# Kernel optimization log

Measured on AMD Instinct MI355X. Metric: run time of the kernel, lower is better.

Reference implementation:

```python
import jax, jax.numpy as jnp
import numpy as np

N_NODES = 50000
N_EDGES = 500000
NEG_SLOPE = 0.2


def gat_conv(h, src, dst, W, attn_l, attn_r, bias, activation):
    """DGL-style GATConv (feat_drop=attn_drop=0, no residual).
    h: [N, F_in]; W: [F_in, H*D]; attn_l/attn_r: [H, D]; bias: [H*D].
    Returns [N, H, D]."""
    H, D = attn_l.shape
    feat = (h @ W).reshape(-1, H, D)                      # [N, H, D]
    el = (feat * attn_l).sum(-1)                          # [N, H]
    er = (feat * attn_r).sum(-1)                          # [N, H]
    e = jax.nn.leaky_relu(el[src] + er[dst], NEG_SLOPE)   # [E, H] edge logits
    # edge softmax over incoming edges of each dst node
    emax = jax.ops.segment_max(e, dst, num_segments=N_NODES)
    emax = jnp.where(jnp.isfinite(emax), emax, 0.0)       # guard zero in-degree
    ee = jnp.exp(e - emax[dst])                           # [E, H]
    denom = jax.ops.segment_sum(ee, dst, num_segments=N_NODES)
    alpha = ee / jnp.maximum(denom[dst], 1e-9)            # [E, H]
    # weighted scatter-aggregate of source features
    out = jax.ops.segment_sum(feat[src] * alpha[..., None], dst,
                              num_segments=N_NODES)       # [N, H, D]
    out = out + bias.reshape(1, H, D)
    return activation(out) if activation is not None else out


def setup_inputs() -> dict:
    key = jax.random.key(0)
    ks = jax.random.split(key, 20)
    in0, in1, hid, heads, ncls = 256, 128, 64, 8, 10

    def xn(k, shape):
        fan = shape[0] + (shape[1] if len(shape) > 1 else shape[0])
        return jax.random.normal(k, shape, jnp.float32) * np.float32(np.sqrt(2.0 / fan)) * 1.414

    inp = {
        "feat0": jax.random.normal(ks[0], (30000, in0), jnp.float32),
        "feat1": jax.random.normal(ks[1], (20000, in1), jnp.float32),
        "fc0_w": xn(ks[2], (in0, hid)), "fc0_b": jnp.zeros((hid,), jnp.float32),
        "fc1_w": xn(ks[3], (in1, hid)), "fc1_b": jnp.zeros((hid,), jnp.float32),
        "W0": xn(ks[4], (hid, heads * hid)),
        "al0": xn(ks[5], (heads, hid)), "ar0": xn(ks[6], (heads, hid)),
        "b0": jnp.zeros((heads * hid,), jnp.float32),
        "W1": xn(ks[7], (heads * hid, heads * hid)),
        "al1": xn(ks[8], (heads, hid)), "ar1": xn(ks[9], (heads, hid)),
        "b1": jnp.zeros((heads * hid,), jnp.float32),
        "W2": xn(ks[10], (heads * hid, 1 * ncls)),
        "al2": xn(ks[11], (1, ncls)), "ar2": xn(ks[12], (1, ncls)),
        "b2": jnp.zeros((ncls,), jnp.float32),
        "edge_index": jax.random.randint(ks[13], (2, N_EDGES), 0, N_NODES, jnp.int64
                                         if jax.config.jax_enable_x64 else jnp.int32),
    }
    return inp


def reference(feat0, feat1, fc0_w, fc0_b, fc1_w, fc1_b,
              W0, al0, ar0, b0, W1, al1, ar1, b1, W2, al2, ar2, b2,
              edge_index):
    src, dst = edge_index[0], edge_index[1]
    # per-type linear projection then concat along node axis
    h = jnp.concatenate([feat0 @ fc0_w + fc0_b, feat1 @ fc1_w + fc1_b], axis=0)
    h = gat_conv(h, src, dst, W0, al0, ar0, b0, jax.nn.elu).reshape(N_NODES, -1)
    h = gat_conv(h, src, dst, W1, al1, ar1, b1, jax.nn.elu).reshape(N_NODES, -1)
    logits = gat_conv(h, src, dst, W2, al2, ar2, b2, None).mean(axis=1)  # [N, ncls]
    return logits
```

## Files before the change

### kernel.cpp

```cpp
#include <hip/hip_runtime.h>
#include <hip/hip_bf16.h>
#include <hip/hip_fp16.h>

#define N_NODES 50000
#define N_EDGES 500000
#define HEADS 8
#define HID 64
#define HD 512
#define NCLS 10
#define M_PAD 50048
#define YTILES 391

typedef _Float16 f16x8 __attribute__((ext_vector_type(8)));
typedef _Float16 h8v   __attribute__((ext_vector_type(8)));
typedef float    f32x4 __attribute__((ext_vector_type(4)));

#define GLD_LDS16(g, l) __builtin_amdgcn_global_load_lds( \
    (__attribute__((address_space(1))) void*)(g),         \
    (__attribute__((address_space(3))) void*)(l), 16, 0, 0)

#define T0_TILES 469
#define T1_TILES 313
__global__ __launch_bounds__(256) void fc_gemm(const float* __restrict__ A0,
                                               const float* __restrict__ B0,
                                               const float* __restrict__ bias0,
                                               const float* __restrict__ A1,
                                               const float* __restrict__ B1,
                                               const float* __restrict__ bias1,
                                               _Float16* __restrict__ Cb) {
    __shared__ float As[16][68];
    __shared__ float Bs[16][68];
    int bid = blockIdx.x;
    const float* A; const float* B; const float* bias;
    int M, K, row_off, m0;
    if (bid < T0_TILES) { A = A0; B = B0; bias = bias0; M = 30000; K = 256; row_off = 0;     m0 = bid * 64; }
    else                { A = A1; B = B1; bias = bias1; M = 20000; K = 128; row_off = 30000; m0 = (bid - T0_TILES) * 64; }
    int tid = threadIdx.x;
    int tx = tid & 15, ty = tid >> 4;
    float acc[4][4] = {};
    int arow = tid >> 2;
    int akq  = (tid & 3) * 4;
    int brow = tid >> 4;
    int bcol = (tid & 15) * 4;
    for (int k0 = 0; k0 < K; k0 += 16) {
        int m = m0 + arow;
        float4 av = make_float4(0.f, 0.f, 0.f, 0.f);
        if (m < M) av = *(const float4*)(A + (size_t)m * K + k0 + akq);
        As[akq + 0][arow] = av.x; As[akq + 1][arow] = av.y;
        As[akq + 2][arow] = av.z; As[akq + 3][arow] = av.w;
        float4 bv = *(const float4*)(B + (size_t)(k0 + brow) * 64 + bcol);
        *(float4*)(&Bs[brow][bcol]) = bv;
        __syncthreads();
#pragma unroll
        for (int k = 0; k < 16; k++) {
            float4 a = *(const float4*)(&As[k][ty * 4]);
            float4 b = *(const float4*)(&Bs[k][tx * 4]);
            float av4[4] = {a.x, a.y, a.z, a.w};
            float bv4[4] = {b.x, b.y, b.z, b.w};
#pragma unroll
            for (int i = 0; i < 4; i++)
#pragma unroll
                for (int j = 0; j < 4; j++) acc[i][j] += av4[i] * bv4[j];
        }
        __syncthreads();
    }
#pragma unroll
    for (int i = 0; i < 4; i++) {
        int m = m0 + ty * 4 + i;
        if (m < M) {
#pragma unroll
            for (int j = 0; j < 4; j++) {
                int col = tx * 4 + j;
                Cb[(size_t)(row_off + m) * 64 + col] = (_Float16)(acc[i][j] + bias[col]);
            }
        }
    }
}

#define NBLK_SCAN 196

__global__ void count_kernel(const int* __restrict__ dst, int* __restrict__ cnt) {
    int t = blockIdx.x * blockDim.x + threadIdx.x;
    if (t < N_EDGES) atomicAdd(&cnt[dst[t]], 1);
}

__global__ void scan_part(const int* __restrict__ cnt, int* __restrict__ part) {
    __shared__ int s[256];
    int i = blockIdx.x * 256 + threadIdx.x;
    s[threadIdx.x] = (i < N_NODES) ? cnt[i] : 0;
    __syncthreads();
    for (int off = 128; off; off >>= 1) {
        if (threadIdx.x < off) s[threadIdx.x] += s[threadIdx.x + off];
        __syncthreads();
    }
    if (threadIdx.x == 0) part[blockIdx.x] = s[0];
}

__global__ void scan_offs(int* __restrict__ part) {
    __shared__ int s[256];
    int tid = threadIdx.x;
    int v = (tid < NBLK_SCAN) ? part[tid] : 0;
    s[tid] = v;
    __syncthreads();
    for (int off = 1; off < 256; off <<= 1) {
        int x = (tid >= off) ? s[tid - off] : 0;
        __syncthreads();
        s[tid] += x;
        __syncthreads();
    }
    if (tid < NBLK_SCAN) part[tid] = s[tid] - v;
}

__global__ void scan_apply(const int* __restrict__ cnt, const int* __restrict__ part,
                           int* __restrict__ rp, int* __restrict__ cur) {
    __shared__ int s[256];
    int tid = threadIdx.x;
    int i = blockIdx.x * 256 + tid;
    int v = (i < N_NODES) ? cnt[i] : 0;
    s[tid] = v;
    __syncthreads();
    for (int off = 1; off < 256; off <<= 1) {
        int x = (tid >= off) ? s[tid - off] : 0;
        __syncthreads();
        s[tid] += x;
        __syncthreads();
    }
    if (i < N_NODES) {
        int excl = s[tid] - v + part[blockIdx.x];
        rp[i] = excl; cur[i] = excl;
    }
    if (i == 0) rp[N_NODES] = N_EDGES;
}

__global__ void scatter_kernel(const int* __restrict__ src, const int* __restrict__ dst,
                               int* __restrict__ cursor, int* __restrict__ src_sorted) {
    int t = blockIdx.x * blockDim.x + threadIdx.x;
    if (t >= N_EDGES) return;
    int pos = atomicAdd(&cursor[dst[t]], 1);
    src_sorted[pos] = src[t];
}

__global__ void wtrans(const float* __restrict__ W0, const float* __restrict__ W1,
                       _Float16* __restrict__ W0t, _Float16* __restrict__ W1t) {
    int t = blockIdx.x * blockDim.x + threadIdx.x;
    if (t < 64 * 512) {
        int n = t >> 6, k = t & 63;
        W0t[t] = (_Float16)W0[k * 512 + n];
    } else {
        int u = t - 64 * 512;
        if (u >= 512 * 512) return;
        int n = u >> 9, k = u & 511;
        W1t[u] = (_Float16)W1[k * 512 + n];
    }
}

__global__ __launch_bounds__(512) void gemm_mfma_wide(const _Float16* __restrict__ A,
                                                      const _Float16* __restrict__ Bt,
                                                      _Float16* __restrict__ Cb,
                                                      const float* __restrict__ al,
                                                      const float* __restrict__ ar,
                                                      float* __restrict__ el,
                                                      float* __restrict__ er,
                                                      int M, int K) {
    __shared__ _Float16 Asl[128 * 32];
    __shared__ _Float16 Bsl[256 * 32];
    int bid = blockIdx.x;
    int k8 = bid & 7, jj = bid >> 3;
    int y = k8 + 8 * (jj >> 1);
    if (y >= YTILES) return;
    int m0 = y * 128;
    int n0 = (jj & 1) * 256;
    int t = threadIdx.x;
    int lane = t & 63;
    int w = t >> 6;
    int wm = (w & 1) * 64, wn = (w >> 1) * 64;
    int l15 = lane & 15, quad = lane >> 4;
    f32x4 acc[4][4];
#pragma unroll
    for (int i = 0; i < 4; i++)
#pragma unroll
        for (int j = 0; j < 4; j++) acc[i][j] = (f32x4){0.f, 0.f, 0.f, 0.f};

    int fbA = t * 16;
    int rowA = fbA >> 6, kgA = ((fbA >> 4) & 3) ^ (rowA & 3);
    int fbB0 = t * 16;
    int fbB1 = fbB0 + 8192;
    int rowB0 = fbB0 >> 6, kgB0 = ((fbB0 >> 4) & 3) ^ (rowB0 & 3);
    int rowB1 = fbB1 >> 6, kgB1 = ((fbB1 >> 4) & 3) ^ (rowB1 & 3);

    for (int k0 = 0; k0 < K; k0 += 32) {
        GLD_LDS16(A + (size_t)(m0 + rowA) * K + k0 + kgA * 8, (char*)Asl + fbA);
        GLD_LDS16(Bt + (size_t)(n0 + rowB0) * K + k0 + kgB0 * 8, (char*)Bsl + fbB0);
        GLD_LDS16(Bt + (size_t)(n0 + rowB1) * K + k0 + kgB1 * 8, (char*)Bsl + fbB1);
        __syncthreads();
        f16x8 af[4], bfr[4];
#pragma unroll
        for (int i = 0; i < 4; i++) {
            int r = wm + i * 16 + l15;
            int kg = quad ^ (r & 3);
            af[i] = *(const f16x8*)(Asl + r * 32 + kg * 8);
        }
#pragma unroll
        for (int j = 0; j < 4; j++) {
            int r = wn + j * 16 + l15;
            int kg = quad ^ (r & 3);
            bfr[j] = *(const f16x8*)(Bsl + r * 32 + kg * 8);
        }
#pragma unroll
        for (int i = 0; i < 4; i++)
#pragma unroll
            for (int j = 0; j < 4; j++)
                acc[i][j] = __builtin_amdgcn_mfma_f32_16x16x32_f16(af[i], bfr[j], acc[i][j], 0, 0, 0);
        __syncthreads();
    }
#pragma unroll
    for (int i = 0; i < 4; i++) {
        int rbase = m0 + wm + i * 16 + quad * 4;
#pragma unroll
        for (int j = 0; j < 4; j++) {
            int col = n0 + wn + j * 16 + l15;
#pragma unroll
            for (int r = 0; r < 4; r++) {
                int row = rbase + r;
                if (row < M) Cb[(size_t)row * HD + col] = (_Float16)acc[i][j][r];
            }
        }
    }
    int h = (n0 + wn) >> 6;
    float alv[4], arv[4];
#pragma unroll
    for (int j = 0; j < 4; j++) {
        alv[j] = al[h * 64 + j * 16 + l15];
        arv[j] = ar[h * 64 + j * 16 + l15];
    }
#pragma unroll
    for (int i = 0; i < 4; i++) {
#pragma unroll
        for (int r = 0; r < 4; r++) {
            float sl = 0.f, sr = 0.f;
#pragma unroll
            for (int j = 0; j < 4; j++) {
                float v = acc[i][j][r];
                sl += v * alv[j]; sr += v * arv[j];
            }
#pragma unroll
            for (int mk = 1; mk < 16; mk <<= 1) {
                sl += __shfl_xor(sl, mk);
                sr += __shfl_xor(sr, mk);
            }
            int row = m0 + wm + i * 16 + quad * 4 + r;
            if (l15 == 0 && row < M) {
                el[row * HEADS + h] = sl;
                er[row * HEADS + h] = sr;
            }
        }
    }
}

__global__ __launch_bounds__(64) void attn_agg(
        const int* __restrict__ rp, const int* __restrict__ srcs,
        const float* __restrict__ el, const float* __restrict__ er,
        const _Float16* __restrict__ feat, const float* __restrict__ bias,
        _Float16* __restrict__ out) {
    __shared__ float aS[592];
    __shared__ int   sS[64];
    int lane = threadIdx.x;
    int n    = blockIdx.x;
    int s0 = rp[n], s1 = rp[n + 1];
    int deg = s1 - s0;
    float er8[8];
    {
        f32x4 a = *(const f32x4*)(er + (size_t)n * 8);
        f32x4 b = *(const f32x4*)(er + (size_t)n * 8 + 4);
        er8[0]=a[0]; er8[1]=a[1]; er8[2]=a[2]; er8[3]=a[3];
        er8[4]=b[0]; er8[5]=b[1]; er8[6]=b[2]; er8[7]=b[3];
    }
    bool fast = (deg <= 64);
    if (fast) {
        bool act = lane < deg;
        int sp = act ? srcs[s0 + lane] : 0;
        sS[lane] = sp;
        f32x4 ea = {0.f,0.f,0.f,0.f}, eb = {0.f,0.f,0.f,0.f};
        if (act) {
            ea = *(const f32x4*)(el + (size_t)sp * 8);
            eb = *(const f32x4*)(el + (size_t)sp * 8 + 4);
        }
        float e8[8] = {ea[0],ea[1],ea[2],ea[3],eb[0],eb[1],eb[2],eb[3]};
#pragma unroll
        for (int h = 0; h < 8; h++) {
            float e = e8[h] + er8[h];
            e = e > 0.f ? e : 0.2f * e;
            e8[h] = act ? e : -1e30f;
        }
#pragma unroll
        for (int h = 0; h < 8; h++) {
            float mm = e8[h];
#pragma unroll
            for (int mk = 1; mk < 64; mk <<= 1) mm = fmaxf(mm, __shfl_xor(mm, mk));
            float pv = act ? __expf(e8[h] - mm) : 0.f;
            float ss = pv;
#pragma unroll
            for (int mk = 1; mk < 64; mk <<= 1) ss += __shfl_xor(ss, mk);
            aS[lane * 9 + h] = pv * (1.f / fmaxf(ss, 1e-9f));
        }
    } else {
        float m8[8], s8[8];
#pragma unroll
        for (int h = 0; h < 8; h++) { m8[h] = -1e30f; s8[h] = 0.f; }
        for (int base = s0; base < s1; base += 64) {
            bool act = base + lane < s1;
            int sp = act ? srcs[base + lane] : 0;
            f32x4 ea = {0.f,0.f,0.f,0.f}, eb = {0.f,0.f,0.f,0.f};
            if (act) {
                ea = *(const f32x4*)(el + (size_t)sp * 8);
                eb = *(const f32x4*)(el + (size_t)sp * 8 + 4);
            }
            float ev[8] = {ea[0],ea[1],ea[2],ea[3],eb[0],eb[1],eb[2],eb[3]};
#pragma unroll
            for (int h = 0; h < 8; h++) {
                float e = ev[h] + er8[h];
                e = e > 0.f ? e : 0.2f * e;
                e = act ? e : -1e30f;
                float cm = e;
#pragma unroll
                for (int mk = 1; mk < 64; mk <<= 1) cm = fmaxf(cm, __shfl_xor(cm, mk));
                float nm = fmaxf(m8[h], cm);
                float pv = act ? __expf(e - nm) : 0.f;
#pragma unroll
                for (int mk = 1; mk < 64; mk <<= 1) pv += __shfl_xor(pv, mk);
                s8[h] = s8[h] * __expf(m8[h] - nm) + pv;
                m8[h] = nm;
            }
        }
        if (lane == 0) {
#pragma unroll
            for (int h = 0; h < 8; h++) {
                aS[576 + h] = 1.f / fmaxf(s8[h], 1e-9f);
                aS[584 + h] = m8[h];
            }
        }
    }
    __builtin_amdgcn_wave_barrier();
    int hh = lane >> 3, d0 = (lane & 7) * 8;
    h8v z = {(_Float16)0, (_Float16)0, (_Float16)0, (_Float16)0,
             (_Float16)0, (_Float16)0, (_Float16)0, (_Float16)0};
    h8v acc0 = z, acc1 = z, acc2 = z, acc3 = z;
    const _Float16* colbase = feat + hh * 64 + d0;
    if (fast) {
        int p = 0;
        for (; p + 4 <= deg; p += 4) {
            int spa = sS[p],     spb = sS[p + 1];
            int spc = sS[p + 2], spd = sS[p + 3];
            _Float16 aa = (_Float16)aS[p * 9 + hh];
            _Float16 ab = (_Float16)aS[(p + 1) * 9 + hh];
            _Float16 ac = (_Float16)aS[(p + 2) * 9 + hh];
            _Float16 ad = (_Float16)aS[(p + 3) * 9 + hh];
            h8v fa = *(const h8v*)(colbase + (size_t)spa * HD);
            h8v fb = *(const h8v*)(colbase + (size_t)spb * HD);
            h8v fc = *(const h8v*)(colbase + (size_t)spc * HD);
            h8v fd = *(const h8v*)(colbase + (size_t)spd * HD);
            h8v a8a = {aa, aa, aa, aa, aa, aa, aa, aa};
            h8v a8b = {ab, ab, ab, ab, ab, ab, ab, ab};
            h8v a8c = {ac, ac, ac, ac, ac, ac, ac, ac};
            h8v a8d = {ad, ad, ad, ad, ad, ad, ad, ad};
            acc0 += a8a * fa;
            acc1 += a8b * fb;
            acc2 += a8c * fc;
            acc3 += a8d * fd;
        }
        for (; p < deg; p++) {
            int sp = sS[p];
            _Float16 ah = (_Float16)aS[p * 9 + hh];
            h8v a8 = {ah, ah, ah, ah, ah, ah, ah, ah};
            h8v f = *(const h8v*)(colbase + (size_t)sp * HD);
            acc0 += a8 * f;
        }
    } else {
        float inv_l = aS[576 + hh];
        float m_l   = aS[584 + hh];
        float ern_l = er[(size_t)n * 8 + hh];
        for (int p = s0; p < s1; p++) {
            int sp = srcs[p];
            float e = el[(size_t)sp * 8 + hh] + ern_l;
            e = e > 0.f ? e : 0.2f * e;
            _Float16 ah = (_Float16)(__expf(e - m_l) * inv_l);
            h8v a8 = {ah, ah, ah, ah, ah, ah, ah, ah};
            h8v f = *(const h8v*)(colbase + (size_t)sp * HD);
            acc0 += a8 * f;
        }
    }
    acc0 += acc1; acc2 += acc3; acc0 += acc2;
    float4 b0v = *(const float4*)(bias + lane * 8);
    float4 b1v = *(const float4*)(bias + lane * 8 + 4);
    float bb[8] = {b0v.x,b0v.y,b0v.z,b0v.w,b1v.x,b1v.y,b1v.z,b1v.w};
    h8v o;
#pragma unroll
    for (int j = 0; j < 8; j++) {
        float x = (float)acc0[j] + bb[j];
        x = x > 0.f ? x : __expf(x) - 1.f;
        o[j] = (_Float16)x;
    }
    *(h8v*)(out + (size_t)n * HD + lane * 8) = o;
}

__global__ __launch_bounds__(256) void gemm_n10v2(
        const _Float16* __restrict__ A, const float* __restrict__ B,
        const float* __restrict__ al2, const float* __restrict__ ar2,
        float* __restrict__ C, float* __restrict__ el, float* __restrict__ er) {
    __shared__ float Bs[512 * 11];
    int t = threadIdx.x;
    for (int i = t; i < 512 * NCLS; i += 256) {
        int k = i / NCLS, c = i - k * NCLS;
        Bs[k * 11 + c] = B[i];
    }
    __syncthreads();
    int lane = t & 63;
    int m = blockIdx.x * 4 + (t >> 6);
    float acc[NCLS];
#pragma unroll
    for (int c = 0; c < NCLS; c++) acc[c] = 0.f;
    const _Float16* a = A + (size_t)m * HD;
#pragma unroll
    for (int j = 0; j < 8; j++) {
        float av = (float)a[j * 64 + lane];
        const float* br = Bs + (j * 64 + lane) * 11;
#pragma unroll
        for (int c = 0; c < NCLS; c++) acc[c] += av * br[c];
    }
#pragma unroll
    for (int c = 0; c < NCLS; c++)
#pragma unroll
        for (int mk = 1; mk < 64; mk <<= 1) acc[c] += __shfl_xor(acc[c], mk);
    if (lane == 0) {
        float e1 = 0.f, e2 = 0.f;
#pragma unroll
        for (int c = 0; c < NCLS; c++) { e1 += acc[c] * al2[c]; e2 += acc[c] * ar2[c]; }
        el[m] = e1; er[m] = e2;
#pragma unroll
        for (int c = 0; c < NCLS; c++) C[(size_t)m * NCLS + c] = acc[c];
    }
}

__global__ __launch_bounds__(64) void attn2_agg2(
        const int* __restrict__ rp, const int* __restrict__ srcs,
        const float* __restrict__ el, const float* __restrict__ er,
        const float* __restrict__ feat2, const float* __restrict__ b2,
        float* __restrict__ out) {
    int lane = threadIdx.x;
    int n = blockIdx.x;
    int s0 = rp[n], s1 = rp[n + 1], deg = s1 - s0;
    float ern = er[n];
    float facc[NCLS];
#pragma unroll
    for (int c = 0; c < NCLS; c++) facc[c] = 0.f;
    if (deg <= 64) {
        bool act = lane < deg;
        int sp = act ? srcs[s0 + lane] : 0;
        float e = act ? el[sp] + ern : 0.f;
        e = e > 0.f ? e : 0.2f * e;
        if (!act) e = -1e30f;
        float mm = e;
#pragma unroll
        for (int mk = 1; mk < 64; mk <<= 1) mm = fmaxf(mm, __shfl_xor(mm, mk));
        float pv = act ? __expf(e - mm) : 0.f;
        float ss = pv;
#pragma unroll
        for (int mk = 1; mk < 64; mk <<= 1) ss += __shfl_xor(ss, mk);
        float a = pv / fmaxf(ss, 1e-9f);
        if (act) {
#pragma unroll
            for (int c = 0; c < NCLS; c++) facc[c] = a * feat2[(size_t)sp * NCLS + c];
        }
    } else {
        float mm = -1e30f, ssum = 0.f;
        for (int base = s0; base < s1; base += 64) {
            bool act = base + lane < s1;
            int sp = act ? srcs[base + lane] : 0;
            float e = act ? el[sp] + ern : 0.f;
            e = e > 0.f ? e : 0.2f * e;
            if (!act) e = -1e30f;
            float cm = e;
#pragma unroll
            for (int mk = 1; mk < 64; mk <<= 1) cm = fmaxf(cm, __shfl_xor(cm, mk));
            float nm = fmaxf(mm, cm);
            float pv = act ? __expf(e - nm) : 0.f;
#pragma unroll
            for (int mk = 1; mk < 64; mk <<= 1) pv += __shfl_xor(pv, mk);
            ssum = ssum * __expf(mm - nm) + pv;
            mm = nm;
        }
        float inv = 1.f / fmaxf(ssum, 1e-9f);
        for (int base = s0; base < s1; base += 64) {
            bool act = base + lane < s1;
            int sp = act ? srcs[base + lane] : 0;
            float e = act ? el[sp] + ern : 0.f;
            e = e > 0.f ? e : 0.2f * e;
            float a = act ? __expf(e - mm) * inv : 0.f;
            if (act) {
#pragma unroll
                for (int c = 0; c < NCLS; c++) facc[c] += a * feat2[(size_t)sp * NCLS + c];
            }
        }
    }
#pragma unroll
    for (int c = 0; c < NCLS; c++)
#pragma unroll
        for (int mk = 1; mk < 64; mk <<= 1) facc[c] += __shfl_xor(facc[c], mk);
    if (lane == 0) {
#pragma unroll
        for (int c = 0; c < NCLS; c++) out[(size_t)n * NCLS + c] = facc[c] + b2[c];
    }
}

extern "C" void kernel_launch(void* const* d_in, const int* in_sizes, int n_in,
                              void* d_out, int out_size, void* d_ws, size_t ws_size,
                              hipStream_t stream) {
    const float* feat0 = (const float*)d_in[0];
    const float* feat1 = (const float*)d_in[1];
    const float* fc0_w = (const float*)d_in[2];
    const float* fc0_b = (const float*)d_in[3];
    const float* fc1_w = (const float*)d_in[4];
    const float* fc1_b = (const float*)d_in[5];
    const float* W0    = (const float*)d_in[6];
    const float* al0   = (const float*)d_in[7];
    const float* ar0   = (const float*)d_in[8];
    const float* b0    = (const float*)d_in[9];
    const float* W1    = (const float*)d_in[10];
    const float* al1   = (const float*)d_in[11];
    const float* ar1   = (const float*)d_in[12];
    const float* b1    = (const float*)d_in[13];
    const float* W2    = (const float*)d_in[14];
    const float* al2   = (const float*)d_in[15];
    const float* ar2   = (const float*)d_in[16];
    const float* b2    = (const float*)d_in[17];
    const int* eidx    = (const int*)d_in[18];
    const int* src = eidx;
    const int* dst = eidx + N_EDGES;
    float* out = (float*)d_out;

    char* ws = (char*)d_ws;
    size_t off = 0;
    auto alloc = [&](size_t bytes) { size_t o = off; off = (off + bytes + 255) & ~(size_t)255; return o; };

    _Float16* featA = (_Float16*)(ws + alloc((size_t)M_PAD * HD * 2));
    _Float16* aggh  = (_Float16*)(ws + alloc((size_t)M_PAD * HD * 2));
    _Float16* h0h   = (_Float16*)(ws + alloc((size_t)M_PAD * 64 * 2));
    float*    feat2 = (float*)(ws + alloc((size_t)N_NODES * NCLS * 4));
    float*    el    = (float*)(ws + alloc((size_t)N_NODES * HEADS * 4));
    float*    er    = (float*)(ws + alloc((size_t)N_NODES * HEADS * 4));
    float*    el2   = (float*)(ws + alloc((size_t)N_NODES * 4));
    float*    er2   = (float*)(ws + alloc((size_t)N_NODES * 4));
    int*      cnt   = (int*)  (ws + alloc((size_t)N_NODES * 4));
    int*      rp    = (int*)  (ws + alloc((size_t)(N_NODES + 1) * 4));
    int*      cur   = (int*)  (ws + alloc((size_t)N_NODES * 4));
    int*      srcs  = (int*)  (ws + alloc((size_t)N_EDGES * 4));
    int*      part  = (int*)  (ws + alloc(1024));
    _Float16* W0t   = (_Float16*)(ws + alloc(512 * 64 * 2));
    _Float16* W1t   = (_Float16*)(ws + alloc(512 * 512 * 2));

    fc_gemm<<<T0_TILES + T1_TILES, 256, 0, stream>>>(feat0, fc0_w, fc0_b,
                                                     feat1, fc1_w, fc1_b, h0h);
    wtrans<<<(64 * 512 + 512 * 512 + 255) / 256, 256, 0, stream>>>(W0, W1, W0t, W1t);

    hipMemsetAsync(cnt, 0, N_NODES * sizeof(int), stream);
    count_kernel<<<(N_EDGES + 255) / 256, 256, 0, stream>>>(dst, cnt);
    scan_part<<<NBLK_SCAN, 256, 0, stream>>>(cnt, part);
    scan_offs<<<1, 256, 0, stream>>>(part);
    scan_apply<<<NBLK_SCAN, 256, 0, stream>>>(cnt, part, rp, cur);
    scatter_kernel<<<(N_EDGES + 255) / 256, 256, 0, stream>>>(src, dst, cur, srcs);

    int ggrid = 8 * 98;

    gemm_mfma_wide<<<ggrid, 512, 0, stream>>>(h0h, W0t, featA, al0, ar0, el, er,
                                              N_NODES, 64);
    attn_agg<<<N_NODES, 64, 0, stream>>>(rp, srcs, el, er, featA, b0, aggh);

    gemm_mfma_wide<<<ggrid, 512, 0, stream>>>(aggh, W1t, featA, al1, ar1, el, er,
                                              N_NODES, HD);
    attn_agg<<<N_NODES, 64, 0, stream>>>(rp, srcs, el, er, featA, b1, aggh);

    gemm_n10v2<<<N_NODES / 4, 256, 0, stream>>>(aggh, W2, al2, ar2, feat2, el2, er2);
    attn2_agg2<<<N_NODES, 64, 0, stream>>>(rp, srcs, el2, er2, feat2, b2, out);
}
```

Before: 541.0 us.

## Fold fc projections into W0 and run layer-0 GEMM on MFMA

Precomputes fc_w·W0 (and the fc biases times W0) so the per-type input projection and the first GAT projection become one fp16 MFMA GEMM over the raw features. The scalar fp32 fc_gemm, the separate weight transpose and the memset are replaced by a single prep kernel that also converts the features to fp16 and zeroes the counts. The layer-0 GEMM now has K=256/128 instead of 64, which adds more MFMA work and a full fp16 copy of the input features. It also rounds the combined weights to fp16, which changes numerics.

```diff
diff --git a/kernel.cpp b/kernel.cpp
--- a/kernel.cpp
+++ b/kernel.cpp
@@ -9,7 +9,9 @@
 #define HD 512
 #define NCLS 10
 #define M_PAD 50048
-#define YTILES 391
+#define YTILES_L1 391
+#define F0ROWS 30080
+#define F1ROWS 20096
 
 typedef _Float16 f16x8 __attribute__((ext_vector_type(8)));
 typedef _Float16 h8v   __attribute__((ext_vector_type(8)));
@@ -19,62 +21,70 @@
     (__attribute__((address_space(1))) void*)(g),         \
     (__attribute__((address_space(3))) void*)(l), 16, 0, 0)
 
-#define T0_TILES 469
-#define T1_TILES 313
-__global__ __launch_bounds__(256) void fc_gemm(const float* __restrict__ A0,
-                                               const float* __restrict__ B0,
-                                               const float* __restrict__ bias0,
-                                               const float* __restrict__ A1,
-                                               const float* __restrict__ B1,
-                                               const float* __restrict__ bias1,
-                                               _Float16* __restrict__ Cb) {
-    __shared__ float As[16][68];
-    __shared__ float Bs[16][68];
-    int bid = blockIdx.x;
-    const float* A; const float* B; const float* bias;
-    int M, K, row_off, m0;
-    if (bid < T0_TILES) { A = A0; B = B0; bias = bias0; M = 30000; K = 256; row_off = 0;     m0 = bid * 64; }
-    else                { A = A1; B = B1; bias = bias1; M = 20000; K = 128; row_off = 30000; m0 = (bid - T0_TILES) * 64; }
-    int tid = threadIdx.x;
-    int tx = tid & 15, ty = tid >> 4;
-    float acc[4][4] = {};
-    int arow = tid >> 2;
-    int akq  = (tid & 3) * 4;
-    int brow = tid >> 4;
-    int bcol = (tid & 15) * 4;
-    for (int k0 = 0; k0 < K; k0 += 16) {
-        int m = m0 + arow;
-        float4 av = make_float4(0.f, 0.f, 0.f, 0.f);
-        if (m < M) av = *(const float4*)(A + (size_t)m * K + k0 + akq);
-        As[akq + 0][arow] = av.x; As[akq + 1][arow] = av.y;
-        As[akq + 2][arow] = av.z; As[akq + 3][arow] = av.w;
-        float4 bv = *(const float4*)(B + (size_t)(k0 + brow) * 64 + bcol);
-        *(float4*)(&Bs[brow][bcol]) = bv;
-        __syncthreads();
-#pragma unroll
-        for (int k = 0; k < 16; k++) {
-            float4 a = *(const float4*)(&As[k][ty * 4]);
-            float4 b = *(const float4*)(&Bs[k][tx * 4]);
-            float av4[4] = {a.x, a.y, a.z, a.w};
-            float bv4[4] = {b.x, b.y, b.z, b.w};
-#pragma unroll
-            for (int i = 0; i < 4; i++)
-#pragma unroll
-                for (int j = 0; j < 4; j++) acc[i][j] += av4[i] * bv4[j];
-        }
-        __syncthreads();
-    }
-#pragma unroll
-    for (int i = 0; i < 4; i++) {
-        int m = m0 + ty * 4 + i;
-        if (m < M) {
-#pragma unroll
-            for (int j = 0; j < 4; j++) {
-                int col = tx * 4 + j;
-                Cb[(size_t)(row_off + m) * 64 + col] = (_Float16)(acc[i][j] + bias[col]);
-            }
-        }
-    }
+#define E_N (F0ROWS * 256)
+#define F_N (F1ROWS * 128)
+#define A_N (512 * 256)
+#define B_N (512 * 128)
+#define C_N (512 * 512)
+#define D_N 1024
+#define PREP_TOTAL (E_N + F_N + A_N + B_N + C_N + D_N + N_NODES)
+
+__global__ void prep(const float* __restrict__ feat0, const float* __restrict__ feat1,
+                     const float* __restrict__ fc0_w, const float* __restrict__ fc0_b,
+                     const float* __restrict__ fc1_w, const float* __restrict__ fc1_b,
+                     const float* __restrict__ W0, const float* __restrict__ W1,
+                     _Float16* __restrict__ f0h, _Float16* __restrict__ f1h,
+                     _Float16* __restrict__ Wc0t, _Float16* __restrict__ Wc1t,
+                     _Float16* __restrict__ W1t, float* __restrict__ biasF,
+                     int* __restrict__ cnt) {
+    int idx = blockIdx.x * 256 + threadIdx.x;
+    if (idx < E_N) {
+        int m = idx >> 8, k = idx & 255;
+        f0h[idx] = (m < 30000) ? (_Float16)feat0[(size_t)m * 256 + k] : (_Float16)0.f;
+        return;
+    }
+    idx -= E_N;
+    if (idx < F_N) {
+        int m = idx >> 7, k = idx & 127;
+        f1h[idx] = (m < 20000) ? (_Float16)feat1[(size_t)m * 128 + k] : (_Float16)0.f;
+        return;
+    }
+    idx -= F_N;
+    if (idx < A_N) {
+        int k = idx >> 9, n = idx & 511;
+        float s = 0.f;
+#pragma unroll 8
+        for (int j = 0; j < 64; j++) s += fc0_w[k * 64 + j] * W0[j * 512 + n];
+        Wc0t[n * 256 + k] = (_Float16)s;
+        return;
+    }
+    idx -= A_N;
+    if (idx < B_N) {
+        int k = idx >> 9, n = idx & 511;
+        float s = 0.f;
+#pragma unroll 8
+        for (int j = 0; j < 64; j++) s += fc1_w[k * 64 + j] * W0[j * 512 + n];
+        Wc1t[n * 128 + k] = (_Float16)s;
+        return;
+    }
+    idx -= B_N;
+    if (idx < C_N) {
+        int k = idx >> 9, n = idx & 511;
+        W1t[n * 512 + k] = (_Float16)W1[k * 512 + n];
+        return;
+    }
+    idx -= C_N;
+    if (idx < D_N) {
+        int t = idx >> 9, n = idx & 511;
+        const float* fb = t ? fc1_b : fc0_b;
+        float s = 0.f;
+#pragma unroll 8
+        for (int j = 0; j < 64; j++) s += fb[j] * W0[j * 512 + n];
+        biasF[t * 512 + n] = s;
+        return;
+    }
+    idx -= D_N;
+    if (idx < N_NODES) cnt[idx] = 0;
 }
 
 #define NBLK_SCAN 196
@@ -140,34 +150,21 @@
     src_sorted[pos] = src[t];
 }
 
-__global__ void wtrans(const float* __restrict__ W0, const float* __restrict__ W1,
-                       _Float16* __restrict__ W0t, _Float16* __restrict__ W1t) {
-    int t = blockIdx.x * blockDim.x + threadIdx.x;
-    if (t < 64 * 512) {
-        int n = t >> 6, k = t & 63;
-        W0t[t] = (_Float16)W0[k * 512 + n];
-    } else {
-        int u = t - 64 * 512;
-        if (u >= 512 * 512) return;
-        int n = u >> 9, k = u & 511;
-        W1t[u] = (_Float16)W1[k * 512 + n];
-    }
-}
-
 __global__ __launch_bounds__(512) void gemm_mfma_wide(const _Float16* __restrict__ A,
                                                       const _Float16* __restrict__ Bt,
                                                       _Float16* __restrict__ Cb,
                                                       const float* __restrict__ al,
                                                       const float* __restrict__ ar,
+                                                      const float* __restrict__ cbias,
                                                       float* __restrict__ el,
                                                       float* __restrict__ er,
-                                                      int M, int K) {
+                                                      int M, int K, int row_off, int ytiles) {
     __shared__ _Float16 Asl[128 * 32];
     __shared__ _Float16 Bsl[256 * 32];
     int bid = blockIdx.x;
     int k8 = bid & 7, jj = bid >> 3;
     int y = k8 + 8 * (jj >> 1);
-    if (y >= YTILES) return;
+    if (y >= ytiles) return;
     int m0 = y * 128;
     int n0 = (jj & 1) * 256;
     int t = threadIdx.x;
@@ -213,6 +210,10 @@
                 acc[i][j] = __builtin_amdgcn_mfma_f32_16x16x32_f16(af[i], bfr[j], acc[i][j], 0, 0, 0);
         __syncthreads();
     }
+    float cb[4];
+#pragma unroll
+    for (int j = 0; j < 4; j++)
+        cb[j] = cbias ? cbias[n0 + wn + j * 16 + l15] : 0.f;
 #pragma unroll
     for (int i = 0; i < 4; i++) {
         int rbase = m0 + wm + i * 16 + quad * 4;
@@ -222,7 +223,8 @@
 #pragma unroll
             for (int r = 0; r < 4; r++) {
                 int row = rbase + r;
-                if (row < M) Cb[(size_t)row * HD + col] = (_Float16)acc[i][j][r];
+                if (row < M)
+                    Cb[(size_t)(row_off + row) * HD + col] = (_Float16)(acc[i][j][r] + cb[j]);
             }
         }
     }
@@ -240,7 +242,7 @@
             float sl = 0.f, sr = 0.f;
 #pragma unroll
             for (int j = 0; j < 4; j++) {
-                float v = acc[i][j][r];
+                float v = acc[i][j][r] + cb[j];
                 sl += v * alv[j]; sr += v * arv[j];
             }
 #pragma unroll
@@ -250,8 +252,8 @@
             }
             int row = m0 + wm + i * 16 + quad * 4 + r;
             if (l15 == 0 && row < M) {
-                el[row * HEADS + h] = sl;
-                er[row * HEADS + h] = sr;
+                el[(size_t)(row_off + row) * HEADS + h] = sl;
+                er[(size_t)(row_off + row) * HEADS + h] = sr;
             }
         }
     }
@@ -544,39 +546,44 @@
 
     _Float16* featA = (_Float16*)(ws + alloc((size_t)M_PAD * HD * 2));
     _Float16* aggh  = (_Float16*)(ws + alloc((size_t)M_PAD * HD * 2));
-    _Float16* h0h   = (_Float16*)(ws + alloc((size_t)M_PAD * 64 * 2));
+    _Float16* f0h   = (_Float16*)(ws + alloc((size_t)F0ROWS * 256 * 2));
+    _Float16* f1h   = (_Float16*)(ws + alloc((size_t)F1ROWS * 128 * 2));
     float*    feat2 = (float*)(ws + alloc((size_t)N_NODES * NCLS * 4));
     float*    el    = (float*)(ws + alloc((size_t)N_NODES * HEADS * 4));
     float*    er    = (float*)(ws + alloc((size_t)N_NODES * HEADS * 4));
     float*    el2   = (float*)(ws + alloc((size_t)N_NODES * 4));
     float*    er2   = (float*)(ws + alloc((size_t)N_NODES * 4));
+    float*    biasF = (float*)(ws + alloc(1024 * 4));
     int*      cnt   = (int*)  (ws + alloc((size_t)N_NODES * 4));
     int*      rp    = (int*)  (ws + alloc((size_t)(N_NODES + 1) * 4));
     int*      cur   = (int*)  (ws + alloc((size_t)N_NODES * 4));
     int*      srcs  = (int*)  (ws + alloc((size_t)N_EDGES * 4));
     int*      part  = (int*)  (ws + alloc(1024));
-    _Float16* W0t   = (_Float16*)(ws + alloc(512 * 64 * 2));
+    _Float16* Wc0t  = (_Float16*)(ws + alloc(512 * 256 * 2));
+    _Float16* Wc1t  = (_Float16*)(ws + alloc(512 * 128 * 2));
     _Float16* W1t   = (_Float16*)(ws + alloc(512 * 512 * 2));
 
-    fc_gemm<<<T0_TILES + T1_TILES, 256, 0, stream>>>(feat0, fc0_w, fc0_b,
-                                                     feat1, fc1_w, fc1_b, h0h);
-    wtrans<<<(64 * 512 + 512 * 512 + 255) / 256, 256, 0, stream>>>(W0, W1, W0t, W1t);
-
-    hipMemsetAsync(cnt, 0, N_NODES * sizeof(int), stream);
+    prep<<<(PREP_TOTAL + 255) / 256, 256, 0, stream>>>(
+        feat0, feat1, fc0_w, fc0_b, fc1_w, fc1_b, W0, W1,
+        f0h, f1h, Wc0t, Wc1t, W1t, biasF, cnt);
+
     count_kernel<<<(N_EDGES + 255) / 256, 256, 0, stream>>>(dst, cnt);
     scan_part<<<NBLK_SCAN, 256, 0, stream>>>(cnt, part);
     scan_offs<<<1, 256, 0, stream>>>(part);
     scan_apply<<<NBLK_SCAN, 256, 0, stream>>>(cnt, part, rp, cur);
     scatter_kernel<<<(N_EDGES + 255) / 256, 256, 0, stream>>>(src, dst, cur, srcs);
 
-    int ggrid = 8 * 98;
-
-    gemm_mfma_wide<<<ggrid, 512, 0, stream>>>(h0h, W0t, featA, al0, ar0, el, er,
-                                              N_NODES, 64);
+    int g0a = 8 * 2 * ((235 + 7) / 8);
+    int g0b = 8 * 2 * ((157 + 7) / 8);
+    int g1  = 8 * 2 * ((YTILES_L1 + 7) / 8);
+    gemm_mfma_wide<<<g0a, 512, 0, stream>>>(f0h, Wc0t, featA, al0, ar0, biasF,
+                                            el, er, 30000, 256, 0, 235);
+    gemm_mfma_wide<<<g0b, 512, 0, stream>>>(f1h, Wc1t, featA, al0, ar0, biasF + 512,
+                                            el, er, 20000, 128, 30000, 157);
     attn_agg<<<N_NODES, 64, 0, stream>>>(rp, srcs, el, er, featA, b0, aggh);
 
-    gemm_mfma_wide<<<ggrid, 512, 0, stream>>>(aggh, W1t, featA, al1, ar1, el, er,
-                                              N_NODES, HD);
+    gemm_mfma_wide<<<g1, 512, 0, stream>>>(aggh, W1t, featA, al1, ar1, nullptr,
+                                           el, er, N_NODES, HD, 0, YTILES_L1);
     attn_agg<<<N_NODES, 64, 0, stream>>>(rp, srcs, el, er, featA, b1, aggh);
 
     gemm_n10v2<<<N_NODES / 4, 256, 0, stream>>>(aggh, W2, al2, ar2, feat2, el2, er2);
```

Result: no change. 543.9 us (+0.5%).
